# Kernel optimization log

Hardware: AMD Instinct MI355X
Metric: run time of the kernel (lower is better)

Reference implementation:

```python
import jax, jax.numpy as jnp
import numpy as np

N = 30000
NUM_FEAT = 129   # data.x.shape[1] + 1
NUM_CLASSES = 40
HID = 64

def _gat_conv(x, src, dst, W, a_src, a_dst, bias):
    """PyG GATConv (concat=True, negative_slope=0.2), self-loops pre-added to src/dst."""
    n = x.shape[0]
    H, C = a_src.shape
    h = (x @ W).reshape(n, H, C)                       # [N,H,C]
    alpha_s = jnp.sum(h * a_src[None], axis=-1)        # [N,H]
    alpha_d = jnp.sum(h * a_dst[None], axis=-1)        # [N,H]
    e = jax.nn.leaky_relu(alpha_s[src] + alpha_d[dst], 0.2)   # [E,H]
    m = jax.ops.segment_max(e, dst, num_segments=n)
    m = jnp.where(jnp.isfinite(m), m, 0.0)
    ex = jnp.exp(e - m[dst])
    denom = jax.ops.segment_sum(ex, dst, num_segments=n)
    alpha = ex / (denom[dst] + 1e-16)                  # segment softmax over in-edges
    out = jax.ops.segment_sum(h[src] * alpha[:, :, None], dst, num_segments=n)
    return out.reshape(n, H * C) + bias


def setup_inputs() -> dict:
    key = jax.random.key(0)
    ks = jax.random.split(key, 16)
    E = 480000
    x = jax.random.normal(ks[0], (N, NUM_FEAT), dtype=jnp.float32)
    edge_index = jax.random.randint(ks[1], (2, E), 0, N, dtype=jnp.int64)
    def w(k, shape, fan_in):
        return (jax.random.normal(k, shape, dtype=jnp.float32) * (1.0 / np.sqrt(fan_in))).astype(jnp.float32)
    # conv1: in=129, H=7, C=64
    W1 = w(ks[2], (NUM_FEAT, 7 * HID), NUM_FEAT)
    a1s = w(ks[3], (7, HID), HID); a1d = w(ks[4], (7, HID), HID)
    b1 = jnp.zeros((7 * HID,), jnp.float32)
    # conv2: in=448, H=6, C=64
    W2 = w(ks[5], (7 * HID, 6 * HID), 7 * HID)
    a2s = w(ks[6], (6, HID), HID); a2d = w(ks[7], (6, HID), HID)
    b2 = jnp.zeros((6 * HID,), jnp.float32)
    # conv3: in=384, H=6, C=40
    W3 = w(ks[8], (6 * HID, 6 * NUM_CLASSES), 6 * HID)
    a3s = w(ks[9], (6, NUM_CLASSES), NUM_CLASSES); a3d = w(ks[10], (6, NUM_CLASSES), NUM_CLASSES)
    b3 = jnp.zeros((6 * NUM_CLASSES,), jnp.float32)
    return {"x": x, "edge_index": edge_index,
            "W1": W1, "a1s": a1s, "a1d": a1d, "b1": b1,
            "W2": W2, "a2s": a2s, "a2d": a2d, "b2": b2,
            "W3": W3, "a3s": a3s, "a3d": a3d, "b3": b3}


def reference(x, edge_index, W1, a1s, a1d, b1, W2, a2s, a2d, b2, W3, a3s, a3d, b3):
    n = x.shape[0]
    loop = jnp.arange(n, dtype=edge_index.dtype)
    src = jnp.concatenate([edge_index[0], loop])   # PyG add_self_loops=True
    dst = jnp.concatenate([edge_index[1], loop])
    # dropout is identity in eval mode
    h = _gat_conv(x, src, dst, W1, a1s, a1d, b1)
    h = jax.nn.relu(h)
    h = _gat_conv(h, src, dst, W2, a2s, a2d, b2)
    h = jax.nn.relu(h)
    out = _gat_conv(h, src, dst, W3, a3s, a3d, b3)
    return out
```

## Files before the change

kernel.cpp:

```cpp
#include <hip/hip_runtime.h>
#include <hip/hip_bf16.h>


#define NFEAT 129
#define MPAD  30080
#define BLKSH 11
#define KPD   16

typedef __attribute__((ext_vector_type(8))) short short8v;
typedef __attribute__((ext_vector_type(8))) unsigned short u16x8;
typedef __attribute__((ext_vector_type(8))) __bf16 bf16x8;
typedef __attribute__((ext_vector_type(4))) float f32x4;
typedef unsigned short u16;

union FragU { short8v s; bf16x8 b; };

__device__ inline u16 f2bf(float x) {
    unsigned u = __builtin_bit_cast(unsigned, x);
    unsigned r = (u + 0x7fffu + ((u >> 16) & 1u)) >> 16;
    return (u16)r;
}
__device__ inline float bf2f(u16 b) {
    unsigned u = ((unsigned)b) << 16;
    return __builtin_bit_cast(float, u);
}
__device__ inline float h2f(u16 u) { return (float)__builtin_bit_cast(_Float16, u); }
__device__ inline u16 f2h(float v) { return __builtin_bit_cast(u16, (_Float16)v); }


__global__ __launch_bounds__(256) void hist_k(const int* __restrict__ src,
                                              const int* __restrict__ dst,
                                              int* __restrict__ cnt, int E, int n) {
    int e = blockIdx.x * 256 + threadIdx.x;
    if (e < E + n) {
        int s, d;
        if (e < E) { s = src[e]; d = dst[e]; }
        else       { s = d = e - E; }
        atomicAdd(&cnt[d * KPD + (s >> BLKSH)], 1);
    }
}

__global__ __launch_bounds__(256) void bsum_k(const int* __restrict__ cnt,
                                              int* __restrict__ bsum, int nk) {
    __shared__ int sh[256];
    int t = threadIdx.x, idx = blockIdx.x * 256 + t;
    sh[t] = (idx < nk) ? cnt[idx] : 0;
    __syncthreads();
    for (int o = 128; o; o >>= 1) {
        if (t < o) sh[t] += sh[t + o];
        __syncthreads();
    }
    if (t == 0) bsum[blockIdx.x] = sh[0];
}

__global__ __launch_bounds__(1024) void bscan_k(const int* __restrict__ bsum,
                                                int* __restrict__ bofs, int nb) {
    __shared__ int part[1024];
    int t = threadIdx.x;
    int per = (nb + 1023) >> 10;
    int base = t * per;
    int s = 0;
    for (int j = 0; j < per; ++j) {
        int i = base + j;
        if (i < nb) s += bsum[i];
    }
    part[t] = s;
    __syncthreads();
    for (int o = 1; o < 1024; o <<= 1) {
        int v = 0;
        if (t >= o) v = part[t - o];
        __syncthreads();
        if (t >= o) part[t] += v;
        __syncthreads();
    }
    int run = (t > 0) ? part[t - 1] : 0;
    for (int j = 0; j < per; ++j) {
        int i = base + j;
        if (i < nb) { bofs[i] = run; run += bsum[i]; }
    }
    if (t == 1023) bofs[nb] = part[1023];
}

__global__ __launch_bounds__(256) void scanw_k(const int* __restrict__ cnt,
                                               const int* __restrict__ bofs,
                                               int* __restrict__ row_ptr, int nk) {
    __shared__ int sh[256];
    int t = threadIdx.x, idx = blockIdx.x * 256 + t;
    int v = (idx < nk) ? cnt[idx] : 0;
    sh[t] = v;
    __syncthreads();
    for (int o = 1; o < 256; o <<= 1) {
        int u = 0;
        if (t >= o) u = sh[t - o];
        __syncthreads();
        if (t >= o) sh[t] += u;
        __syncthreads();
    }
    if (idx < nk) row_ptr[idx] = bofs[blockIdx.x] + sh[t] - v;
    if (idx == nk - 1) row_ptr[nk] = bofs[blockIdx.x] + sh[t];
}

__global__ __launch_bounds__(256) void scatter_k(const int* __restrict__ src, const int* __restrict__ dst,
                                                 const int* __restrict__ row_ptr, int* __restrict__ fill,
                                                 int* __restrict__ col, int* __restrict__ dstc,
                                                 int E, int n) {
    int e = blockIdx.x * 256 + threadIdx.x;
    if (e < E + n) {
        int s, d;
        if (e < E) { s = src[e]; d = dst[e]; }
        else       { s = d = e - E; }
        int key = d * KPD + (s >> BLKSH);
        int pos = row_ptr[key] + atomicAdd(&fill[key], 1);
        col[pos] = s;
        dstc[pos] = d;
    }
}


__global__ __launch_bounds__(256) void xsplit_k(const float* __restrict__ in,
                                                u16* __restrict__ hi, u16* __restrict__ lo,
                                                int Nn, int K, int Kp, int Mp) {
    int idx = blockIdx.x * 256 + threadIdx.x;
    if (idx >= Mp * Kp) return;
    int m = idx / Kp, k = idx - m * Kp;
    float v = (m < Nn && k < K) ? in[(size_t)m * K + k] : 0.f;
    u16 h = f2bf(v);
    hi[idx] = h;
    lo[idx] = f2bf(v - bf2f(h));
}


__global__ __launch_bounds__(256) void wsplitAll_k(const float* __restrict__ W1,
                                                   const float* __restrict__ W2,
                                                   const float* __restrict__ W3,
                                                   u16* __restrict__ hi, u16* __restrict__ lo) {
    int idx = blockIdx.x * 256 + threadIdx.x;
    if (idx >= 352256) return;
    const float* W; int loc, Kp, K, N;
    if (idx < 81920)       { W = W1; loc = idx;          Kp = 160; K = 129; N = 448; }
    else if (idx < 253952) { W = W2; loc = idx - 81920;  Kp = 448; K = 448; N = 384; }
    else                   { W = W3; loc = idx - 253952; Kp = 384; K = 384; N = 240; }
    int nn = loc / Kp, k = loc - nn * Kp;
    float v = (k < K && nn < N) ? W[(size_t)k * N + nn] : 0.f;
    u16 h = f2bf(v);
    hi[idx] = h;
    lo[idx] = f2bf(v - bf2f(h));
}


__global__ __launch_bounds__(256) void projAll_k(
    const float* __restrict__ W1, const float* __restrict__ a1s, const float* __restrict__ a1d,
    const float* __restrict__ W2, const float* __restrict__ a2s, const float* __restrict__ a2d,
    const float* __restrict__ W3, const float* __restrict__ a3s, const float* __restrict__ a3d,
    float* __restrict__ Ps, float* __restrict__ Pd) {
    int idx = blockIdx.x * 256 + threadIdx.x;
    if (idx >= 992 * 8) return;
    int row = idx >> 3, h = idx & 7;
    const float *W, *as_, *ad_; int k, K, Ncols, H, C;
    if (row < 160)      { k = row;       K = 129; W = W1; as_ = a1s; ad_ = a1d; Ncols = 448; H = 7; C = 64; }
    else if (row < 608) { k = row - 160; K = 448; W = W2; as_ = a2s; ad_ = a2d; Ncols = 384; H = 6; C = 64; }
    else                { k = row - 608; K = 384; W = W3; as_ = a3s; ad_ = a3d; Ncols = 240; H = 6; C = 40; }
    float ps = 0.f, pd = 0.f;
    if (h < H && k < K) {
        const float* wr = W + (size_t)k * Ncols + h * C;
        const float* ar = as_ + h * C;
        const float* dr = ad_ + h * C;
        for (int c = 0; c < C; ++c) {
            float wv = wr[c];
            ps += wv * ar[c];
            pd += wv * dr[c];
        }
    }
    Ps[idx] = ps;
    Pd[idx] = pd;
}


__global__ __launch_bounds__(256) void zeropads_k(u16* __restrict__ h1hi, u16* __restrict__ h1lo,
                                                  int Nn) {
    int tot = (MPAD - Nn) * 448;
    int idx = blockIdx.x * 256 + threadIdx.x;
    if (idx < tot) {
        h1hi[(size_t)Nn * 448 + idx] = 0;
        h1lo[(size_t)Nn * 448 + idx] = 0;
    }
}


__global__ __launch_bounds__(256) void alpha1_k(const float* __restrict__ x,
                                                const float* __restrict__ Ps,
                                                const float* __restrict__ Pd,
                                                float* __restrict__ oS, float* __restrict__ oD, int n) {
    int wv = threadIdx.x >> 6, lane = threadIdx.x & 63;
    int i = blockIdx.x * 4 + wv;
    if (i >= n) return;
    const float* row = x + (size_t)i * NFEAT;
    float x0 = row[lane], x1 = row[64 + lane];
    float ps[8], pd[8];
    #pragma unroll
    for (int h = 0; h < 8; ++h) {
        ps[h] = x0 * Ps[lane * 8 + h] + x1 * Ps[(64 + lane) * 8 + h];
        pd[h] = x0 * Pd[lane * 8 + h] + x1 * Pd[(64 + lane) * 8 + h];
    }
    if (lane == 0) {
        float x2 = row[128];
        #pragma unroll
        for (int h = 0; h < 8; ++h) {
            ps[h] += x2 * Ps[128 * 8 + h];
            pd[h] += x2 * Pd[128 * 8 + h];
        }
    }
    #pragma unroll
    for (int h = 0; h < 8; ++h) {
        #pragma unroll
        for (int off = 32; off; off >>= 1) {
            ps[h] += __shfl_xor(ps[h], off);
            pd[h] += __shfl_xor(pd[h], off);
        }
    }
    if (lane == 0) {
        #pragma unroll
        for (int h = 0; h < 8; ++h) {
            oS[(size_t)i * 8 + h] = ps[h];
            oD[(size_t)i * 8 + h] = pd[h];
        }
    }
}


template <int KC>
__global__ __launch_bounds__(256) void alphaproj_k(const u16* __restrict__ Hhi,
                                                   const u16* __restrict__ Hlo,
                                                   const float* __restrict__ Ps,
                                                   const float* __restrict__ Pd,
                                                   float* __restrict__ oS, float* __restrict__ oD, int n) {
    constexpr int STRIDE = KC * 64;
    int wv = threadIdx.x >> 6, lane = threadIdx.x & 63;
    int i = blockIdx.x * 4 + wv;
    if (i >= n) return;
    const u16* bh = Hhi + (size_t)i * STRIDE;
    const u16* bl = Hlo + (size_t)i * STRIDE;
    float ps[8] = {}, pd[8] = {};
    #pragma unroll
    for (int kc = 0; kc < KC; ++kc) {
        int k = kc * 64 + lane;
        float v = bf2f(bh[k]) + bf2f(bl[k]);
        #pragma unroll
        for (int h = 0; h < 8; ++h) {
            ps[h] += v * Ps[k * 8 + h];
            pd[h] += v * Pd[k * 8 + h];
        }
    }
    #pragma unroll
    for (int h = 0; h < 8; ++h) {
        #pragma unroll
        for (int off = 32; off; off >>= 1) {
            ps[h] += __shfl_xor(ps[h], off);
            pd[h] += __shfl_xor(pd[h], off);
        }
    }
    if (lane == 0) {
        #pragma unroll
        for (int h = 0; h < 8; ++h) {
            oS[(size_t)i * 8 + h] = ps[h];
            oD[(size_t)i * 8 + h] = pd[h];
        }
    }
}


__global__ __launch_bounds__(256) void edgew_k(const float* __restrict__ as_,
                                               const float* __restrict__ ad_,
                                               const int* __restrict__ col,
                                               const int* __restrict__ dstc,
                                               float* __restrict__ w, int Et) {
    int idx = blockIdx.x * 256 + threadIdx.x;
    if (idx >= Et * 8) return;
    int e = idx >> 3, h = idx & 7;
    int s = col[e], d = dstc[e];
    float v = as_[(size_t)s * 8 + h] + ad_[(size_t)d * 8 + h];
    v = v > 0.f ? v : 0.2f * v;
    w[idx] = __expf(v);
}


__device__ __forceinline__ int swz(int r, int s) {
    return (r << 2) | ((s ^ (r & 3) ^ ((r >> 2) & 3)) & 3);
}


__global__ __launch_bounds__(256) void gemm16(
    const u16* __restrict__ Ahi, const u16* __restrict__ Alo,
    const u16* __restrict__ Bhi, const u16* __restrict__ Blo,
    u16* __restrict__ C16, int M, int Ncols, int Kp)
{
    __shared__ __align__(16) u16 sAh[128 * 32];
    __shared__ __align__(16) u16 sAl[128 * 32];
    __shared__ __align__(16) u16 sBh[128 * 32];
    __shared__ __align__(16) u16 sBl[128 * 32];
    const int tid = threadIdx.x;
    const int m0 = blockIdx.y * 128;
    const int n0 = blockIdx.x * 128;
    const int lane = tid & 63, wave = tid >> 6;
    const int wm = wave >> 1, wn = wave & 1;
    const int l15 = lane & 15, lg = lane >> 4;
    const int r0 = tid >> 2, s0 = tid & 3;
    const int w0 = swz(r0, s0), w1 = swz(r0 + 64, s0);
    f32x4 acc[4][4] = {};

    for (int k0 = 0; k0 < Kp; k0 += 32) {
        size_t gA0 = (size_t)(m0 + r0) * Kp + k0 + s0 * 8;
        size_t gA1 = (size_t)(m0 + r0 + 64) * Kp + k0 + s0 * 8;
        size_t gB0 = (size_t)(n0 + r0) * Kp + k0 + s0 * 8;
        size_t gB1 = (size_t)(n0 + r0 + 64) * Kp + k0 + s0 * 8;
        short8v ah0 = *(const short8v*)(Ahi + gA0);
        short8v ah1 = *(const short8v*)(Ahi + gA1);
        short8v al0 = *(const short8v*)(Alo + gA0);
        short8v al1 = *(const short8v*)(Alo + gA1);
        short8v bh0 = *(const short8v*)(Bhi + gB0);
        short8v bh1 = *(const short8v*)(Bhi + gB1);
        short8v bl0 = *(const short8v*)(Blo + gB0);
        short8v bl1 = *(const short8v*)(Blo + gB1);
        __syncthreads();
        ((short8v*)sAh)[w0] = ah0; ((short8v*)sAh)[w1] = ah1;
        ((short8v*)sAl)[w0] = al0; ((short8v*)sAl)[w1] = al1;
        ((short8v*)sBh)[w0] = bh0; ((short8v*)sBh)[w1] = bh1;
        ((short8v*)sBl)[w0] = bl0; ((short8v*)sBl)[w1] = bl1;
        __syncthreads();
        FragU fah[4], fal[4], fbh[4], fbl[4];
        #pragma unroll
        for (int mf = 0; mf < 4; ++mf) {
            int rr = wm * 64 + mf * 16 + l15;
            int idx = swz(rr, lg);
            fah[mf].s = ((const short8v*)sAh)[idx];
            fal[mf].s = ((const short8v*)sAl)[idx];
        }
        #pragma unroll
        for (int nf = 0; nf < 4; ++nf) {
            int rr = wn * 64 + nf * 16 + l15;
            int idx = swz(rr, lg);
            fbh[nf].s = ((const short8v*)sBh)[idx];
            fbl[nf].s = ((const short8v*)sBl)[idx];
        }
        #pragma unroll
        for (int mf = 0; mf < 4; ++mf) {
            #pragma unroll
            for (int nf = 0; nf < 4; ++nf) {
                acc[mf][nf] = __builtin_amdgcn_mfma_f32_16x16x32_bf16(fah[mf].b, fbh[nf].b, acc[mf][nf], 0, 0, 0);
                acc[mf][nf] = __builtin_amdgcn_mfma_f32_16x16x32_bf16(fah[mf].b, fbl[nf].b, acc[mf][nf], 0, 0, 0);
                acc[mf][nf] = __builtin_amdgcn_mfma_f32_16x16x32_bf16(fal[mf].b, fbh[nf].b, acc[mf][nf], 0, 0, 0);
            }
        }
    }
    #pragma unroll
    for (int mf = 0; mf < 4; ++mf) {
        #pragma unroll
        for (int nf = 0; nf < 4; ++nf) {
            int colg = n0 + wn * 64 + nf * 16 + l15;
            if (colg >= Ncols) continue;
            #pragma unroll
            for (int r = 0; r < 4; ++r) {
                int rowg = m0 + wm * 64 + mf * 16 + lg * 4 + r;
                if (rowg < M) C16[(size_t)rowg * Ncols + colg] = f2h(acc[mf][nf][r]);
            }
        }
    }
}


template <int H, int C, bool RELU, bool SPLIT>
__global__ __launch_bounds__(256) void aggL_k(
    const u16* __restrict__ hf, const float* __restrict__ w,
    const float* __restrict__ bias,
    const int* __restrict__ row_ptr, const int* __restrict__ col,
    float* __restrict__ outf, u16* __restrict__ ohi, u16* __restrict__ olo, int n)
{
    constexpr int HC = H * C;
    constexpr int LACT = HC / 8;
    const int wv = threadIdx.x >> 6, lane = threadIdx.x & 63;
    const int i = blockIdx.x * 4 + wv;
    if (i >= n) return;
    const int ch0 = lane * 8;
    const bool act = lane < LACT;
    const int h = act ? (ch0 / C) : 0;
    const bool lead = act && ((ch0 % C) == 0);
    const int beg = row_ptr[i * KPD], end = row_ptr[(i + 1) * KPD];
    float acc[8] = {};
    float dp = 0.f;
    if (act) {
        int e = beg;
        for (; e + 2 <= end; e += 2) {
            int sA = col[e], sB = col[e + 1];
            float wA = w[(size_t)e * 8 + h];
            float wB = w[(size_t)(e + 1) * 8 + h];
            u16x8 vA = *(const u16x8*)(hf + (size_t)sA * HC + ch0);
            u16x8 vB = *(const u16x8*)(hf + (size_t)sB * HC + ch0);
            #pragma unroll
            for (int j = 0; j < 8; ++j)
                acc[j] += wA * h2f(vA[j]) + wB * h2f(vB[j]);
            if (lead) dp += wA + wB;
        }
        if (e < end) {
            int sA = col[e];
            float wA = w[(size_t)e * 8 + h];
            u16x8 vA = *(const u16x8*)(hf + (size_t)sA * HC + ch0);
            #pragma unroll
            for (int j = 0; j < 8; ++j)
                acc[j] += wA * h2f(vA[j]);
            if (lead) dp += wA;
        }
    }
    const float den = __shfl(dp, h * (C / 8)) + 1e-16f;
    if (act) {
        float o[8];
        #pragma unroll
        for (int j = 0; j < 8; ++j) {
            float v = acc[j] / den + bias[ch0 + j];
            if (RELU) v = fmaxf(v, 0.f);
            o[j] = v;
        }
        size_t base = (size_t)i * HC + ch0;
        if constexpr (SPLIT) {
            u16x8 ph, pl;
            #pragma unroll
            for (int j = 0; j < 8; ++j) {
                u16 hi = f2bf(o[j]);
                ph[j] = hi;
                pl[j] = f2bf(o[j] - bf2f(hi));
            }
            *(u16x8*)(ohi + base) = ph;
            *(u16x8*)(olo + base) = pl;
        } else {
            float4 q0; q0.x = o[0]; q0.y = o[1]; q0.z = o[2]; q0.w = o[3];
            float4 q1; q1.x = o[4]; q1.y = o[5]; q1.z = o[6]; q1.w = o[7];
            *(float4*)(outf + base) = q0;
            *(float4*)(outf + base + 4) = q1;
        }
    }
}


extern "C" void kernel_launch(void* const* d_in, const int* in_sizes, int n_in,
                              void* d_out, int out_size, void* d_ws, size_t ws_size,
                              hipStream_t stream) {
    const float* x   = (const float*)d_in[0];
    const int*   ei  = (const int*)d_in[1];
    const float* W1  = (const float*)d_in[2];
    const float* a1s = (const float*)d_in[3];
    const float* a1d = (const float*)d_in[4];
    const float* b1  = (const float*)d_in[5];
    const float* W2  = (const float*)d_in[6];
    const float* a2s = (const float*)d_in[7];
    const float* a2d = (const float*)d_in[8];
    const float* b2  = (const float*)d_in[9];
    const float* W3  = (const float*)d_in[10];
    const float* a3s = (const float*)d_in[11];
    const float* a3d = (const float*)d_in[12];
    const float* b3  = (const float*)d_in[13];
    float* out = (float*)d_out;

    const int Nn = in_sizes[0] / NFEAT;
    const int E  = in_sizes[1] / 2;
    const int Et = E + Nn;
    const int NK = Nn * KPD;
    const int NB = (NK + 255) / 256;
    const int* srcp = ei;
    const int* dstp = ei + E;

    char* ws = (char*)d_ws;
    size_t off = 0;
    auto carve = [&](size_t bytes) -> char* {
        char* p = ws + off;
        off += (bytes + 255) & ~(size_t)255;
        return p;
    };
    u16*   hbuf16 = (u16*)carve((size_t)MPAD * 448 * 2);
    u16*   h1hi  = (u16*)carve((size_t)MPAD * 448 * 2);
    u16*   h1lo  = (u16*)carve((size_t)MPAD * 448 * 2);
    u16*   Xhi   = (u16*)carve((size_t)MPAD * 160 * 2);
    u16*   Xlo   = (u16*)carve((size_t)MPAD * 160 * 2);
    u16*   Wthi  = (u16*)carve((size_t)352256 * 2);
    u16*   Wtlo  = (u16*)carve((size_t)352256 * 2);
    float* wbuf  = (float*)carve((size_t)Et * 8 * 4);
    int*   col   = (int*)carve((size_t)Et * 4);
    int*   dstc  = (int*)carve((size_t)Et * 4);
    int* row_ptr = (int*)carve((size_t)(NK + 1) * 4);
    int*   cnt   = (int*)carve((size_t)NK * 4);
    int*   bsum  = (int*)carve((size_t)NB * 4);
    int*   bofs  = (int*)carve((size_t)(NB + 1) * 4);
    float* aA    = (float*)carve((size_t)Nn * 8 * 4);
    float* dA    = (float*)carve((size_t)Nn * 8 * 4);
    float* aB    = (float*)carve((size_t)Nn * 8 * 4);
    float* dB    = (float*)carve((size_t)Nn * 8 * 4);
    float* Ps    = (float*)carve((size_t)992 * 8 * 4);
    float* Pd    = (float*)carve((size_t)992 * 8 * 4);
    (void)ws_size;

    const int nb4 = (Nn + 3) / 4;
    const int mg  = MPAD / 128;

    hipMemsetAsync(cnt, 0, (size_t)NK * 4, stream);
    hist_k<<<(Et + 255) / 256, 256, 0, stream>>>(srcp, dstp, cnt, E, Nn);
    bsum_k<<<NB, 256, 0, stream>>>(cnt, bsum, NK);
    bscan_k<<<1, 1024, 0, stream>>>(bsum, bofs, NB);
    scanw_k<<<NB, 256, 0, stream>>>(cnt, bofs, row_ptr, NK);
    hipMemsetAsync(cnt, 0, (size_t)NK * 4, stream);
    scatter_k<<<(Et + 255) / 256, 256, 0, stream>>>(srcp, dstp, row_ptr, cnt, col, dstc, E, Nn);

    xsplit_k<<<((MPAD * 160) + 255) / 256, 256, 0, stream>>>(x, Xhi, Xlo, Nn, NFEAT, 160, MPAD);
    wsplitAll_k<<<(352256 + 255) / 256, 256, 0, stream>>>(W1, W2, W3, Wthi, Wtlo);
    projAll_k<<<(992 * 8 + 255) / 256, 256, 0, stream>>>(W1, a1s, a1d, W2, a2s, a2d, W3, a3s, a3d, Ps, Pd);
    zeropads_k<<<(((MPAD - Nn) * 448) + 255) / 256, 256, 0, stream>>>(h1hi, h1lo, Nn);

    alpha1_k<<<nb4, 256, 0, stream>>>(x, Ps, Pd, aA, dA, Nn);
    edgew_k<<<(Et * 8 + 255) / 256, 256, 0, stream>>>(aA, dA, col, dstc, wbuf, Et);
    gemm16<<<dim3(4, mg), 256, 0, stream>>>(Xhi, Xlo, Wthi, Wtlo, hbuf16, Nn, 448, 160);
    aggL_k<7, 64, true, true><<<nb4, 256, 0, stream>>>(
        hbuf16, wbuf, b1, row_ptr, col, nullptr, h1hi, h1lo, Nn);
    alphaproj_k<7><<<nb4, 256, 0, stream>>>(h1hi, h1lo, Ps + 1280, Pd + 1280, aB, dB, Nn);

    edgew_k<<<(Et * 8 + 255) / 256, 256, 0, stream>>>(aB, dB, col, dstc, wbuf, Et);
    gemm16<<<dim3(3, mg), 256, 0, stream>>>(h1hi, h1lo, Wthi + 81920, Wtlo + 81920, hbuf16, Nn, 384, 448);
    aggL_k<6, 64, true, true><<<nb4, 256, 0, stream>>>(
        hbuf16, wbuf, b2, row_ptr, col, nullptr, h1hi, h1lo, Nn);
    alphaproj_k<6><<<nb4, 256, 0, stream>>>(h1hi, h1lo, Ps + 4864, Pd + 4864, aA, dA, Nn);

    edgew_k<<<(Et * 8 + 255) / 256, 256, 0, stream>>>(aA, dA, col, dstc, wbuf, Et);
    gemm16<<<dim3(2, mg), 256, 0, stream>>>(h1hi, h1lo, Wthi + 253952, Wtlo + 253952, hbuf16, Nn, 240, 384);
    aggL_k<6, 40, false, false><<<nb4, 256, 0, stream>>>(
        hbuf16, wbuf, b3, row_ptr, col, out, nullptr, nullptr, Nn);
}
```

Measured before the change: 507.0 us.

## Store intermediate activations as fp16 and split to bf16 hi/lo inside GEMM

Layer outputs from the aggregation kernel are now written as a single fp16 buffer instead of two bf16 hi/lo buffers. The GEMM gains a template path that loads fp16 A tiles and splits them into bf16 hi/lo in registers, and alphaproj reads the fp16 buffer directly. This halves activation write and read traffic between layers. The cost is lower precision for the intermediates (fp16 instead of roughly fp32-equivalent split bf16) plus extra conversion ALU work in the GEMM load loop.

Measured after the change: 494.9 us. 2.4% less time.

```diff
diff --git a/kernel.cpp b/kernel.cpp
--- a/kernel.cpp
+++ b/kernel.cpp
@@ -176,14 +176,13 @@
 }
 
 
-__global__ __launch_bounds__(256) void zeropads_k(u16* __restrict__ h1hi, u16* __restrict__ h1lo,
+__global__ __launch_bounds__(256) void zeropads_k(u16* __restrict__ hA, u16* __restrict__ hB,
                                                   int Nn) {
-    int tot = (MPAD - Nn) * 448;
+    int totA = (MPAD - Nn) * 448;
+    int totB = (MPAD - Nn) * 384;
     int idx = blockIdx.x * 256 + threadIdx.x;
-    if (idx < tot) {
-        h1hi[(size_t)Nn * 448 + idx] = 0;
-        h1lo[(size_t)Nn * 448 + idx] = 0;
-    }
+    if (idx < totA) hA[(size_t)Nn * 448 + idx] = 0;
+    if (idx < totB) hB[(size_t)Nn * 384 + idx] = 0;
 }
 
 
@@ -229,8 +228,7 @@
 
 
 template <int KC>
-__global__ __launch_bounds__(256) void alphaproj_k(const u16* __restrict__ Hhi,
-                                                   const u16* __restrict__ Hlo,
+__global__ __launch_bounds__(256) void alphaproj_k(const u16* __restrict__ H16,
                                                    const float* __restrict__ Ps,
                                                    const float* __restrict__ Pd,
                                                    float* __restrict__ oS, float* __restrict__ oD, int n) {
@@ -238,13 +236,12 @@
     int wv = threadIdx.x >> 6, lane = threadIdx.x & 63;
     int i = blockIdx.x * 4 + wv;
     if (i >= n) return;
-    const u16* bh = Hhi + (size_t)i * STRIDE;
-    const u16* bl = Hlo + (size_t)i * STRIDE;
+    const u16* hr = H16 + (size_t)i * STRIDE;
     float ps[8] = {}, pd[8] = {};
     #pragma unroll
     for (int kc = 0; kc < KC; ++kc) {
         int k = kc * 64 + lane;
-        float v = bf2f(bh[k]) + bf2f(bl[k]);
+        float v = h2f(hr[k]);
         #pragma unroll
         for (int h = 0; h < 8; ++h) {
             ps[h] += v * Ps[k * 8 + h];
@@ -289,8 +286,10 @@
 }
 
 
+template <bool ASPLIT>
 __global__ __launch_bounds__(256) void gemm16(
     const u16* __restrict__ Ahi, const u16* __restrict__ Alo,
+    const u16* __restrict__ A16,
     const u16* __restrict__ Bhi, const u16* __restrict__ Blo,
     u16* __restrict__ C16, int M, int Ncols, int Kp)
 {
@@ -313,10 +312,27 @@
         size_t gA1 = (size_t)(m0 + r0 + 64) * Kp + k0 + s0 * 8;
         size_t gB0 = (size_t)(n0 + r0) * Kp + k0 + s0 * 8;
         size_t gB1 = (size_t)(n0 + r0 + 64) * Kp + k0 + s0 * 8;
-        short8v ah0 = *(const short8v*)(Ahi + gA0);
-        short8v ah1 = *(const short8v*)(Ahi + gA1);
-        short8v al0 = *(const short8v*)(Alo + gA0);
-        short8v al1 = *(const short8v*)(Alo + gA1);
+        short8v ah0, ah1, al0, al1;
+        if constexpr (ASPLIT) {
+            ah0 = *(const short8v*)(Ahi + gA0);
+            ah1 = *(const short8v*)(Ahi + gA1);
+            al0 = *(const short8v*)(Alo + gA0);
+            al1 = *(const short8v*)(Alo + gA1);
+        } else {
+            u16x8 a0 = *(const u16x8*)(A16 + gA0);
+            u16x8 a1 = *(const u16x8*)(A16 + gA1);
+            #pragma unroll
+            for (int j = 0; j < 8; ++j) {
+                float f0 = h2f(a0[j]);
+                u16 h0 = f2bf(f0);
+                ah0[j] = (short)h0;
+                al0[j] = (short)f2bf(f0 - bf2f(h0));
+                float f1 = h2f(a1[j]);
+                u16 h1 = f2bf(f1);
+                ah1[j] = (short)h1;
+                al1[j] = (short)f2bf(f1 - bf2f(h1));
+            }
+        }
         short8v bh0 = *(const short8v*)(Bhi + gB0);
         short8v bh1 = *(const short8v*)(Bhi + gB1);
         short8v bl0 = *(const short8v*)(Blo + gB0);
@@ -368,12 +384,12 @@
 }
 
 
-template <int H, int C, bool RELU, bool SPLIT>
+template <int H, int C, bool RELU, bool F16OUT>
 __global__ __launch_bounds__(256) void aggL_k(
     const u16* __restrict__ hf, const float* __restrict__ w,
     const float* __restrict__ bias,
     const int* __restrict__ row_ptr, const int* __restrict__ col,
-    float* __restrict__ outf, u16* __restrict__ ohi, u16* __restrict__ olo, int n)
+    float* __restrict__ outf, u16* __restrict__ oh16, int n)
 {
     constexpr int HC = H * C;
     constexpr int LACT = HC / 8;
@@ -420,16 +436,11 @@
             o[j] = v;
         }
         size_t base = (size_t)i * HC + ch0;
-        if constexpr (SPLIT) {
-            u16x8 ph, pl;
+        if constexpr (F16OUT) {
+            u16x8 po;
             #pragma unroll
-            for (int j = 0; j < 8; ++j) {
-                u16 hi = f2bf(o[j]);
-                ph[j] = hi;
-                pl[j] = f2bf(o[j] - bf2f(hi));
-            }
-            *(u16x8*)(ohi + base) = ph;
-            *(u16x8*)(olo + base) = pl;
+            for (int j = 0; j < 8; ++j) po[j] = f2h(o[j]);
+            *(u16x8*)(oh16 + base) = po;
         } else {
             float4 q0; q0.x = o[0]; q0.y = o[1]; q0.z = o[2]; q0.w = o[3];
             float4 q1; q1.x = o[4]; q1.y = o[5]; q1.z = o[6]; q1.w = o[7];
@@ -475,8 +486,8 @@
         return p;
     };
     u16*   hbuf16 = (u16*)carve((size_t)MPAD * 448 * 2);
-    u16*   h1hi  = (u16*)carve((size_t)MPAD * 448 * 2);
-    u16*   h1lo  = (u16*)carve((size_t)MPAD * 448 * 2);
+    u16*   hA16  = (u16*)carve((size_t)MPAD * 448 * 2);
+    u16*   hB16  = (u16*)carve((size_t)MPAD * 384 * 2);
     u16*   Xhi   = (u16*)carve((size_t)MPAD * 160 * 2);
     u16*   Xlo   = (u16*)carve((size_t)MPAD * 160 * 2);
     u16*   Wthi  = (u16*)carve((size_t)352256 * 2);
@@ -510,23 +521,28 @@
     xsplit_k<<<((MPAD * 160) + 255) / 256, 256, 0, stream>>>(x, Xhi, Xlo, Nn, NFEAT, 160, MPAD);
     wsplitAll_k<<<(352256 + 255) / 256, 256, 0, stream>>>(W1, W2, W3, Wthi, Wtlo);
     projAll_k<<<(992 * 8 + 255) / 256, 256, 0, stream>>>(W1, a1s, a1d, W2, a2s, a2d, W3, a3s, a3d, Ps, Pd);
-    zeropads_k<<<(((MPAD - Nn) * 448) + 255) / 256, 256, 0, stream>>>(h1hi, h1lo, Nn);
+    zeropads_k<<<(((MPAD - Nn) * 448) + 255) / 256, 256, 0, stream>>>(hA16, hB16, Nn);
 
     alpha1_k<<<nb4, 256, 0, stream>>>(x, Ps, Pd, aA, dA, Nn);
     edgew_k<<<(Et * 8 + 255) / 256, 256, 0, stream>>>(aA, dA, col, dstc, wbuf, Et);
-    gemm16<<<dim3(4, mg), 256, 0, stream>>>(Xhi, Xlo, Wthi, Wtlo, hbuf16, Nn, 448, 160);
+    gemm16<true><<<dim3(4, mg), 256, 0, stream>>>(Xhi, Xlo, nullptr, Wthi, Wtlo,
+                                                  hbuf16, Nn, 448, 160);
     aggL_k<7, 64, true, true><<<nb4, 256, 0, stream>>>(
-        hbuf16, wbuf, b1, row_ptr, col, nullptr, h1hi, h1lo, Nn);
-    alphaproj_k<7><<<nb4, 256, 0, stream>>>(h1hi, h1lo, Ps + 1280, Pd + 1280, aB, dB, Nn);
+        hbuf16, wbuf, b1, row_ptr, col, nullptr, hA16, Nn);
+    alphaproj_k<7><<<nb4, 256, 0, stream>>>(hA16, Ps + 1280, Pd + 1280, aB, dB, Nn);
 
     edgew_k<<<(Et * 8 + 255) / 256, 256, 0, stream>>>(aB, dB, col, dstc, wbuf, Et);
-    gemm16<<<dim3(3, mg), 256, 0, stream>>>(h1hi, h1lo, Wthi + 81920, Wtlo + 81920, hbuf16, Nn, 384, 448);
+    gemm16<false><<<dim3(3, mg), 256, 0, stream>>>(nullptr, nullptr, hA16,
+                                                   Wthi + 81920, Wtlo + 81920,
+                                                   hbuf16, Nn, 384, 448);
     aggL_k<6, 64, true, true><<<nb4, 256, 0, stream>>>(
-        hbuf16, wbuf, b2, row_ptr, col, nullptr, h1hi, h1lo, Nn);
-    alphaproj_k<6><<<nb4, 256, 0, stream>>>(h1hi, h1lo, Ps + 4864, Pd + 4864, aA, dA, Nn);
+        hbuf16, wbuf, b2, row_ptr, col, nullptr, hB16, Nn);
+    alphaproj_k<6><<<nb4, 256, 0, stream>>>(hB16, Ps + 4864, Pd + 4864, aA, dA, Nn);
 
     edgew_k<<<(Et * 8 + 255) / 256, 256, 0, stream>>>(aA, dA, col, dstc, wbuf, Et);
-    gemm16<<<dim3(2, mg), 256, 0, stream>>>(h1hi, h1lo, Wthi + 253952, Wtlo + 253952, hbuf16, Nn, 240, 384);
+    gemm16<false><<<dim3(2, mg), 256, 0, stream>>>(nullptr, nullptr, hB16,
+                                                   Wthi + 253952, Wtlo + 253952,
+                                                   hbuf16, Nn, 240, 384);
     aggL_k<6, 40, false, false><<<nb4, 256, 0, stream>>>(
-        hbuf16, wbuf, b3, row_ptr, col, out, nullptr, nullptr, Nn);
-}
+        hbuf16, wbuf, b3, row_ptr, col, out, nullptr, Nn);
+}
```
